# Kernel optimization log

Measured on AMD Instinct MI355X. Metric: run time of the kernel, lower is better.

## Reference

```python
import jax, jax.numpy as jnp
import numpy as np

N_CAPS, R, CIN, COUT = 10, 1152, 8, 16  # digit caps, primary caps (32*6*6), caps dims
B = 256


def setup_inputs() -> dict:
    key = jax.random.key(0)
    k1, k2 = jax.random.split(key)
    x = jax.random.normal(k1, (B, R, CIN), dtype=jnp.float32)
    # learned transform W: [num_capsules, num_route_nodes, in_channels, out_channels]
    W = jax.random.normal(k2, (N_CAPS, R, CIN, COUT), dtype=jnp.float32)
    return {"x": x, "W": W}


def squash(t, axis=-1):
    sq = jnp.sum(t * t, axis=axis, keepdims=True)
    return sq / (1.0 + sq) * t / jnp.sqrt(sq)


def reference(x, W):
    # u_hat = (x[None,:,:,None,:] @ W[:,None]) -> [N_CAPS, B, R, 1, COUT]; squeeze the 1.
    u_hat = jnp.einsum('bri,nrio->nbro', x, W)  # [N, B, R, O]
    # NOTE: the original forward returns v_j INSIDE the routing loop, so exactly one
    # iteration executes: b_ij = 0 => c_ij = softmax(zeros, dim=route) = 1/R (uniform).
    c = 1.0 / u_hat.shape[2]
    s = jnp.sum(c * u_hat, axis=2, keepdims=True)  # [N, B, 1, O]
    v = squash(s, axis=-1)
    return v[:, :, :, None, :]  # [N, B, 1, 1, O] to match torch v_j shape
```

## Files before the change

kernel.cpp:

```cpp
#include <hip/hip_runtime.h>

#define RNODES 1152
#define KDIM 9216
#define COUT 16
#define NCAPS 10
#define WSTRIDE (KDIM*COUT)

#define SPLITS 32
#define STEPS 9
#define MT 16
#define GBLK 512
#define PARTL (MT*COUT*NCAPS)
#define PARTL4 (PARTL/4)

#define XAB_UNITS (16*1152*16)
#define WT_OFF   ((size_t)XAB_UNITS*16)
#define WT_UNITS (NCAPS*1152*16)
#define PART_OFF (WT_OFF + (size_t)WT_UNITS*16)

using bf16x8 = __attribute__((ext_vector_type(8))) short;
using f32x4  = __attribute__((ext_vector_type(4))) float;

__device__ __forceinline__ unsigned short f2bf(float f) {
  unsigned int u = __builtin_bit_cast(unsigned int, f);
  return (unsigned short)((u + 0x8000u) >> 16);
}

__device__ __forceinline__ void pack_store8(unsigned short* dst, const float* v) {
  union { unsigned short us[8]; uint4 q; } t;
#pragma unroll
  for (int i = 0; i < 8; ++i) t.us[i] = f2bf(v[i]);
  *(uint4*)dst = t.q;
}

__global__ __launch_bounds__(256) void caps_convert(const float* __restrict__ x,
                                                    const float* __restrict__ W,
                                                    unsigned short* __restrict__ wsb) {
  const int bx = blockIdx.x, tid = threadIdx.x;
  if (bx < 1152) {
    const int bt = bx / 72;
    const int r  = (bx % 72) * 256 + tid;
    const int kb = r >> 4, br = r & 15;
    const float* src = x + (size_t)(bt * 16 + br) * KDIM + kb * 8;
    float4 v0 = *(const float4*)src;
    float4 v1 = *(const float4*)(src + 4);
    float v[8] = {v0.x, v0.y, v0.z, v0.w, v1.x, v1.y, v1.z, v1.w};
    pack_store8(wsb + ((size_t)bt * 18432 + r) * 8, v);
  } else {
    const int b2 = bx - 1152;
    const int n  = b2 / 72;
    const int r  = (b2 % 72) * 256 + tid;
    const int kb = r >> 4, o = r & 15;
    const float* src = W + (size_t)n * WSTRIDE + (size_t)kb * 128 + o;
    float v[8];
#pragma unroll
    for (int j = 0; j < 8; ++j) v[j] = src[j * 16];
    pack_store8(wsb + (WT_OFF / 2) + ((size_t)n * 18432 + r) * 8, v);
  }
}

__global__ __launch_bounds__(256, 2) void caps_gemm(const unsigned short* __restrict__ xab,
                                                    const unsigned short* __restrict__ wt,
                                                    float* __restrict__ part) {
  const int tid  = threadIdx.x, bid = blockIdx.x;
  const int mt   = bid >> 5;
  const int ks   = bid & 31;
  const int lane = tid & 63;
  const int wv   = tid >> 6;
  const int q    = lane >> 4;
  const int m16  = lane & 15;
  const int kb0  = ks * (STEPS * 4);

  const unsigned short* ap = xab + ((size_t)(mt * 1152 + kb0 + q) * 16 + m16) * 8;
  const unsigned short* bp0, *bp1, *bp2;
  int nt[3];
#pragma unroll
  for (int j = 0; j < 3; ++j) nt[j] = wv * 3 + j;
  {
    const int n0 = nt[0] < NCAPS ? nt[0] : 0;
    const int n1 = nt[1] < NCAPS ? nt[1] : 0;
    const int n2 = nt[2] < NCAPS ? nt[2] : 0;
    bp0 = wt + ((size_t)(n0 * 1152 + kb0 + q) * 16 + m16) * 8;
    bp1 = wt + ((size_t)(n1 * 1152 + kb0 + q) * 16 + m16) * 8;
    bp2 = wt + ((size_t)(n2 * 1152 + kb0 + q) * 16 + m16) * 8;
  }

  f32x4 acc[3];
#pragma unroll
  for (int i = 0; i < 3; ++i) acc[i] = (f32x4){0.f, 0.f, 0.f, 0.f};

  bf16x8 aA[3], aB[3], bA[3][3], bB[3][3];

  auto loadg = [&](bf16x8 (&AF)[3], bf16x8 (&BF)[3][3], int g) {
#pragma unroll
    for (int s = 0; s < 3; ++s) {
      const int off = (g * 3 + s) * 512;
      AF[s]    = *(const bf16x8*)(ap  + off);
      BF[0][s] = *(const bf16x8*)(bp0 + off);
      BF[1][s] = *(const bf16x8*)(bp1 + off);
      BF[2][s] = *(const bf16x8*)(bp2 + off);
    }
  };
  auto mmag = [&](bf16x8 (&AF)[3], bf16x8 (&BF)[3][3]) {
#pragma unroll
    for (int s = 0; s < 3; ++s)
#pragma unroll
      for (int j = 0; j < 3; ++j)
        acc[j] = __builtin_amdgcn_mfma_f32_16x16x32_bf16(AF[s], BF[j][s], acc[j], 0, 0, 0);
  };

  loadg(aA, bA, 0);
  loadg(aB, bB, 1);
  mmag(aA, bA);
  loadg(aA, bA, 2);
  mmag(aB, bB);
  mmag(aA, bA);

  float* P = part + (size_t)bid * PARTL;
#pragma unroll
  for (int j = 0; j < 3; ++j) {
    if (nt[j] < NCAPS) {
#pragma unroll
      for (int r = 0; r < 4; ++r)
        P[nt[j] * (MT * COUT) + (q * 4 + r) * COUT + m16] = acc[j][r];
    }
  }
}

__global__ __launch_bounds__(128, 1) void caps_reduce(const float* __restrict__ ws,
                                                      float* __restrict__ out) {
  const int f  = blockIdx.x * 128 + threadIdx.x;
  const int n  = f >> 10;
  const int b  = (f >> 2) & 255;
  const int o4 = f & 3;
  const int mt = b >> 4, row = b & 15;

  const float4* base = (const float4*)ws + (size_t)(mt * SPLITS) * PARTL4
                       + n * (MT * COUT / 4) + row * 4 + o4;
  float4 s0 = {0,0,0,0}, s1 = {0,0,0,0}, s2 = {0,0,0,0}, s3 = {0,0,0,0};
#pragma unroll
  for (int kk = 0; kk < SPLITS; kk += 4) {
    float4 a0 = base[(size_t)(kk + 0) * PARTL4];
    float4 a1 = base[(size_t)(kk + 1) * PARTL4];
    float4 a2 = base[(size_t)(kk + 2) * PARTL4];
    float4 a3 = base[(size_t)(kk + 3) * PARTL4];
    s0.x += a0.x; s0.y += a0.y; s0.z += a0.z; s0.w += a0.w;
    s1.x += a1.x; s1.y += a1.y; s1.z += a1.z; s1.w += a1.w;
    s2.x += a2.x; s2.y += a2.y; s2.z += a2.z; s2.w += a2.w;
    s3.x += a3.x; s3.y += a3.y; s3.z += a3.z; s3.w += a3.w;
  }
  const float inv = 1.0f / (float)RNODES;
  float4 s;
  s.x = ((s0.x + s1.x) + (s2.x + s3.x)) * inv;
  s.y = ((s0.y + s1.y) + (s2.y + s3.y)) * inv;
  s.z = ((s0.z + s1.z) + (s2.z + s3.z)) * inv;
  s.w = ((s0.w + s1.w) + (s2.w + s3.w)) * inv;

  float sq = s.x * s.x + s.y * s.y + s.z * s.z + s.w * s.w;
  sq += __shfl_xor(sq, 1);
  sq += __shfl_xor(sq, 2);
  const float g = sqrtf(sq) / (1.0f + sq);
  s.x *= g; s.y *= g; s.z *= g; s.w *= g;

  ((float4*)out)[f] = s;
}

extern "C" void kernel_launch(void* const* d_in, const int* in_sizes, int n_in,
                              void* d_out, int out_size, void* d_ws, size_t ws_size,
                              hipStream_t stream) {
  const float* x = (const float*)d_in[0];
  const float* W = (const float*)d_in[1];
  float* out = (float*)d_out;

  unsigned short* wsb  = (unsigned short*)d_ws;
  const unsigned short* xab = (const unsigned short*)d_ws;
  const unsigned short* wt  = (const unsigned short*)((const char*)d_ws + WT_OFF);
  float* part = (float*)((char*)d_ws + PART_OFF);

  caps_convert<<<dim3(1872), dim3(256), 0, stream>>>(x, W, wsb);
  caps_gemm<<<dim3(GBLK), dim3(256), 0, stream>>>(xab, wt, part);
  caps_reduce<<<dim3(80), dim3(128), 0, stream>>>(part, out);
}
```

Before: 75.70 us.

## Fuse split-K GEMM and reduction into one kernel with in-block LDS reduction

Replaces the split-K GEMM plus separate reduce/squash kernel with one kernel. Each 1024-thread block owns one capsule and one 16-row batch tile, and its 16 waves each cover a K slice before being summed in shared memory. Squash is applied in the same block, which removes the partial-sum global round-trip and one launch. In exchange the grid shrinks to 160 large blocks with a single accumulator per wave, and each wave reloads the A tile once per capsule, so occupancy and latency hiding may suffer.

New measurement: 74.75 us. No clear change (-1.3%).

```diff
diff --git a/kernel.cpp b/kernel.cpp
--- a/kernel.cpp
+++ b/kernel.cpp
@@ -6,17 +6,8 @@
 #define NCAPS 10
 #define WSTRIDE (KDIM*COUT)
 
-#define SPLITS 32
-#define STEPS 9
-#define MT 16
-#define GBLK 512
-#define PARTL (MT*COUT*NCAPS)
-#define PARTL4 (PARTL/4)
-
 #define XAB_UNITS (16*1152*16)
 #define WT_OFF   ((size_t)XAB_UNITS*16)
-#define WT_UNITS (NCAPS*1152*16)
-#define PART_OFF (WT_OFF + (size_t)WT_UNITS*16)
 
 using bf16x8 = __attribute__((ext_vector_type(8))) short;
 using f32x4  = __attribute__((ext_vector_type(4))) float;
@@ -59,110 +50,76 @@
   }
 }
 
-__global__ __launch_bounds__(256, 2) void caps_gemm(const unsigned short* __restrict__ xab,
-                                                    const unsigned short* __restrict__ wt,
-                                                    float* __restrict__ part) {
+__global__ __launch_bounds__(1024, 1) void caps_mono(const unsigned short* __restrict__ xab,
+                                                     const unsigned short* __restrict__ wt,
+                                                     float* __restrict__ out) {
+  __shared__ float redbuf[16][256];
+
   const int tid  = threadIdx.x, bid = blockIdx.x;
-  const int mt   = bid >> 5;
-  const int ks   = bid & 31;
+  const int n    = bid >> 4;
+  const int mt   = bid & 15;
+  const int wv   = tid >> 6;
   const int lane = tid & 63;
-  const int wv   = tid >> 6;
   const int q    = lane >> 4;
   const int m16  = lane & 15;
-  const int kb0  = ks * (STEPS * 4);
+  const int kb0  = wv * 72;
 
   const unsigned short* ap = xab + ((size_t)(mt * 1152 + kb0 + q) * 16 + m16) * 8;
-  const unsigned short* bp0, *bp1, *bp2;
-  int nt[3];
-#pragma unroll
-  for (int j = 0; j < 3; ++j) nt[j] = wv * 3 + j;
-  {
-    const int n0 = nt[0] < NCAPS ? nt[0] : 0;
-    const int n1 = nt[1] < NCAPS ? nt[1] : 0;
-    const int n2 = nt[2] < NCAPS ? nt[2] : 0;
-    bp0 = wt + ((size_t)(n0 * 1152 + kb0 + q) * 16 + m16) * 8;
-    bp1 = wt + ((size_t)(n1 * 1152 + kb0 + q) * 16 + m16) * 8;
-    bp2 = wt + ((size_t)(n2 * 1152 + kb0 + q) * 16 + m16) * 8;
-  }
+  const unsigned short* bp = wt  + ((size_t)(n  * 1152 + kb0 + q) * 16 + m16) * 8;
 
-  f32x4 acc[3];
-#pragma unroll
-  for (int i = 0; i < 3; ++i) acc[i] = (f32x4){0.f, 0.f, 0.f, 0.f};
+  f32x4 acc = (f32x4){0.f, 0.f, 0.f, 0.f};
+  bf16x8 aA[3], bA[3], aB[3], bB[3];
 
-  bf16x8 aA[3], aB[3], bA[3][3], bB[3][3];
-
-  auto loadg = [&](bf16x8 (&AF)[3], bf16x8 (&BF)[3][3], int g) {
+  auto loadg = [&](bf16x8 (&A)[3], bf16x8 (&B)[3], int g) {
 #pragma unroll
     for (int s = 0; s < 3; ++s) {
       const int off = (g * 3 + s) * 512;
-      AF[s]    = *(const bf16x8*)(ap  + off);
-      BF[0][s] = *(const bf16x8*)(bp0 + off);
-      BF[1][s] = *(const bf16x8*)(bp1 + off);
-      BF[2][s] = *(const bf16x8*)(bp2 + off);
+      A[s] = *(const bf16x8*)(ap + off);
+      B[s] = *(const bf16x8*)(bp + off);
     }
   };
-  auto mmag = [&](bf16x8 (&AF)[3], bf16x8 (&BF)[3][3]) {
+  auto mmag = [&](bf16x8 (&A)[3], bf16x8 (&B)[3]) {
 #pragma unroll
     for (int s = 0; s < 3; ++s)
-#pragma unroll
-      for (int j = 0; j < 3; ++j)
-        acc[j] = __builtin_amdgcn_mfma_f32_16x16x32_bf16(AF[s], BF[j][s], acc[j], 0, 0, 0);
+      acc = __builtin_amdgcn_mfma_f32_16x16x32_bf16(A[s], B[s], acc, 0, 0, 0);
   };
 
   loadg(aA, bA, 0);
   loadg(aB, bB, 1);
+  mmag(aA, bA); loadg(aA, bA, 2);
+  mmag(aB, bB); loadg(aB, bB, 3);
+  mmag(aA, bA); loadg(aA, bA, 4);
+  mmag(aB, bB); loadg(aB, bB, 5);
   mmag(aA, bA);
-  loadg(aA, bA, 2);
   mmag(aB, bB);
-  mmag(aA, bA);
 
-  float* P = part + (size_t)bid * PARTL;
 #pragma unroll
-  for (int j = 0; j < 3; ++j) {
-    if (nt[j] < NCAPS) {
-#pragma unroll
-      for (int r = 0; r < 4; ++r)
-        P[nt[j] * (MT * COUT) + (q * 4 + r) * COUT + m16] = acc[j][r];
-    }
+  for (int r = 0; r < 4; ++r)
+    redbuf[wv][(q * 4 + r) * 16 + m16] = acc[r];
+  __syncthreads();
+
+  if (tid < 256) {
+    float r0  = redbuf[0][tid],  r1  = redbuf[1][tid];
+    float r2  = redbuf[2][tid],  r3  = redbuf[3][tid];
+    float r4  = redbuf[4][tid],  r5  = redbuf[5][tid];
+    float r6  = redbuf[6][tid],  r7  = redbuf[7][tid];
+    float r8  = redbuf[8][tid],  r9  = redbuf[9][tid];
+    float r10 = redbuf[10][tid], r11 = redbuf[11][tid];
+    float r12 = redbuf[12][tid], r13 = redbuf[13][tid];
+    float r14 = redbuf[14][tid], r15 = redbuf[15][tid];
+    const float lo = ((r0 + r1) + (r2 + r3)) + ((r4 + r5) + (r6 + r7));
+    const float hi = ((r8 + r9) + (r10 + r11)) + ((r12 + r13) + (r14 + r15));
+    const float v  = (lo + hi) * (1.0f / (float)RNODES);
+
+    float sq = v * v;
+    sq += __shfl_xor(sq, 1);
+    sq += __shfl_xor(sq, 2);
+    sq += __shfl_xor(sq, 4);
+    sq += __shfl_xor(sq, 8);
+    const float g = sqrtf(sq) / (1.0f + sq);
+
+    out[n * 4096 + (mt * 16 + (tid >> 4)) * 16 + (tid & 15)] = v * g;
   }
-}
-
-__global__ __launch_bounds__(128, 1) void caps_reduce(const float* __restrict__ ws,
-                                                      float* __restrict__ out) {
-  const int f  = blockIdx.x * 128 + threadIdx.x;
-  const int n  = f >> 10;
-  const int b  = (f >> 2) & 255;
-  const int o4 = f & 3;
-  const int mt = b >> 4, row = b & 15;
-
-  const float4* base = (const float4*)ws + (size_t)(mt * SPLITS) * PARTL4
-                       + n * (MT * COUT / 4) + row * 4 + o4;
-  float4 s0 = {0,0,0,0}, s1 = {0,0,0,0}, s2 = {0,0,0,0}, s3 = {0,0,0,0};
-#pragma unroll
-  for (int kk = 0; kk < SPLITS; kk += 4) {
-    float4 a0 = base[(size_t)(kk + 0) * PARTL4];
-    float4 a1 = base[(size_t)(kk + 1) * PARTL4];
-    float4 a2 = base[(size_t)(kk + 2) * PARTL4];
-    float4 a3 = base[(size_t)(kk + 3) * PARTL4];
-    s0.x += a0.x; s0.y += a0.y; s0.z += a0.z; s0.w += a0.w;
-    s1.x += a1.x; s1.y += a1.y; s1.z += a1.z; s1.w += a1.w;
-    s2.x += a2.x; s2.y += a2.y; s2.z += a2.z; s2.w += a2.w;
-    s3.x += a3.x; s3.y += a3.y; s3.z += a3.z; s3.w += a3.w;
-  }
-  const float inv = 1.0f / (float)RNODES;
-  float4 s;
-  s.x = ((s0.x + s1.x) + (s2.x + s3.x)) * inv;
-  s.y = ((s0.y + s1.y) + (s2.y + s3.y)) * inv;
-  s.z = ((s0.z + s1.z) + (s2.z + s3.z)) * inv;
-  s.w = ((s0.w + s1.w) + (s2.w + s3.w)) * inv;
-
-  float sq = s.x * s.x + s.y * s.y + s.z * s.z + s.w * s.w;
-  sq += __shfl_xor(sq, 1);
-  sq += __shfl_xor(sq, 2);
-  const float g = sqrtf(sq) / (1.0f + sq);
-  s.x *= g; s.y *= g; s.z *= g; s.w *= g;
-
-  ((float4*)out)[f] = s;
 }
 
 extern "C" void kernel_launch(void* const* d_in, const int* in_sizes, int n_in,
@@ -175,9 +132,7 @@
   unsigned short* wsb  = (unsigned short*)d_ws;
   const unsigned short* xab = (const unsigned short*)d_ws;
   const unsigned short* wt  = (const unsigned short*)((const char*)d_ws + WT_OFF);
-  float* part = (float*)((char*)d_ws + PART_OFF);
 
   caps_convert<<<dim3(1872), dim3(256), 0, stream>>>(x, W, wsb);
-  caps_gemm<<<dim3(GBLK), dim3(256), 0, stream>>>(xab, wt, part);
-  caps_reduce<<<dim3(80), dim3(128), 0, stream>>>(part, out);
+  caps_mono<<<dim3(160), dim3(1024), 0, stream>>>(xab, wt, out);
 }
```
